# Kernel tuning notes

Measured on AMD Instinct MI355X. Metric: run time of the kernel, lower is better.

Reference implementation:

```python
import jax, jax.numpy as jnp
import numpy as np

# EEACSF hyperparameters (module defaults)
CUTOFF = 5.2
ANG_CUTOFF = 3.5
RADIAL_ETA = 16.0
ANGULAR_ETA = 8.0
RDIV = 16          # radial_dist_divisions
ADIV = 4           # angular_dist_divisions
ZETA = 32.0
SECTIONS = 4       # angle_sections
R_START = 0.8
A_START = 0.8
N_SPECIES = 87     # size of periodic-table / valence table

N_ATOMS = 20000
N_EDGES = 640000       # radial edges
N_ANG_EDGES = 160000   # angular-graph edges
N_PAIRS = 560000       # angle pairs


def setup_inputs() -> dict:
    key = jax.random.key(0)
    ks = jax.random.split(key, 12)
    species = jax.random.randint(ks[0], (N_ATOMS,), 0, N_SPECIES)
    # radial graph: distances in (R_START, CUTOFF)
    distances = R_START + (CUTOFF - R_START) * jax.random.uniform(ks[1], (N_EDGES,), jnp.float32)
    switch = jax.random.uniform(ks[2], (N_EDGES,), jnp.float32)
    edge_src = jax.random.randint(ks[3], (N_EDGES,), 0, N_ATOMS)
    edge_dst = jax.random.randint(ks[4], (N_EDGES,), 0, N_ATOMS)
    # angular graph
    ang_angles = np.pi * jax.random.uniform(ks[5], (N_PAIRS,), jnp.float32)
    ang_distances = A_START + (ANG_CUTOFF - A_START) * jax.random.uniform(ks[6], (N_ANG_EDGES,), jnp.float32)
    ang_switch = jax.random.uniform(ks[7], (N_ANG_EDGES,), jnp.float32)
    ang_edge_dst = jax.random.randint(ks[8], (N_ANG_EDGES,), 0, N_ATOMS)
    angle_src = jax.random.randint(ks[9], (N_PAIRS,), 0, N_ANG_EDGES)
    angle_dst = jax.random.randint(ks[10], (N_PAIRS,), 0, N_ANG_EDGES)
    central_atom = jax.random.randint(ks[11], (N_PAIRS,), 0, N_ATOMS)
    # valence structure table (stands in for the preprocessed VALENCE_STRUCTURE constant)
    valence_table = jax.random.uniform(jax.random.fold_in(key, 99), (N_SPECIES, 4), jnp.float32)
    return {
        "species": species, "distances": distances, "switch": switch,
        "edge_src": edge_src, "edge_dst": edge_dst,
        "ang_angles": ang_angles, "ang_distances": ang_distances,
        "ang_switch": ang_switch, "ang_edge_dst": ang_edge_dst,
        "angle_src": angle_src, "angle_dst": angle_dst,
        "central_atom": central_atom, "valence_table": valence_table,
    }


def reference(species, distances, switch, edge_src, edge_dst,
              ang_angles, ang_distances, ang_switch, ang_edge_dst,
              angle_src, angle_dst, central_atom, valence_table):
    n_atoms = species.shape[0]
    valence = valence_table[species]                                  # [N,4]

    # ---- radial AEV ----
    shiftR = jnp.asarray(np.linspace(R_START, CUTOFF, RDIV + 1)[None, :-1], distances.dtype)
    x2 = RADIAL_ETA * (distances[:, None] - shiftR) ** 2              # [E,16]
    radial_terms = 0.25 * jnp.exp(-x2) * switch[:, None]              # [E,16]
    radial_aev = jax.ops.segment_sum(
        radial_terms[:, :, None] * valence[edge_dst, None, :],        # [E,16,4]
        edge_src, num_segments=n_atoms,
    ).reshape(n_atoms, -1)                                            # [N,64]

    # ---- angular AEV ----
    d12 = 0.5 * (ang_distances[angle_src] + ang_distances[angle_dst])[:, None]  # [P,1]
    angle_start = np.pi / (2 * SECTIONS)
    shiftZ = jnp.asarray((np.linspace(0, np.pi, SECTIONS + 1) + angle_start)[None, :-1], ang_distances.dtype)
    shiftA = jnp.asarray(np.linspace(A_START, ANG_CUTOFF, ADIV + 1)[None, :-1], ang_distances.dtype)
    factor1 = (0.5 + 0.5 * jnp.cos(ang_angles[:, None] - shiftZ)) ** ZETA       # [P,4]
    factor2 = jnp.exp(-ANGULAR_ETA * (d12 - shiftA) ** 2)                       # [P,4]
    angular_terms = (factor1[:, None, :] * factor2[:, :, None]).reshape(-1, SECTIONS * ADIV)
    angular_terms = angular_terms * 2 * (ang_switch[angle_src] * ang_switch[angle_dst])[:, None]  # [P,16]

    valence_dst = valence[ang_edge_dst]                               # [E2,4]
    vp = valence_dst[angle_src] + valence_dst[angle_dst]              # [P,4]
    vm = valence_dst[angle_src] * valence_dst[angle_dst]              # [P,4]
    valence_ang = (vp[:, :, None] * vm[:, None, :]).reshape(-1, 16)   # [P,16]

    angular_aev = jax.ops.segment_sum(
        angular_terms[:, :, None] * valence_ang[:, None, :],          # [P,16,16]
        central_atom, num_segments=n_atoms,
    ).reshape(n_atoms, -1)                                            # [N,256]

    onehot = jax.nn.one_hot(species, N_SPECIES, dtype=distances.dtype)  # [N,87]
    return jnp.concatenate((onehot, radial_aev, angular_aev), axis=-1)  # [N,407]
```

## Files before the change

kernel.cpp:

```cpp
#include <hip/hip_runtime.h>
#include <hip/hip_fp16.h>
#include <math.h>

#define NCOLS   407
#define RAD_OFF 87
#define ANG_OFF 151
#define T1      2048
#define WB      32
#define MAXBKT  640
#define CAPF    1792


typedef __attribute__((ext_vector_type(8))) _Float16 f16x8;
typedef __attribute__((ext_vector_type(4))) float    f32x4;

static __device__ inline unsigned pack2(float a, float b) {
    __half2 h = __floats2half2_rn(a, b);
    return *reinterpret_cast<unsigned*>(&h);
}
static __device__ inline float2 unpack2(unsigned u) {
    __half2 h = *reinterpret_cast<__half2*>(&u);
    return __half22float2(h);
}

__global__ __launch_bounds__(256) void ze_kernel(const float* __restrict__ ang_dist,
                                                 const float* __restrict__ ang_sw,
                                                 const int* __restrict__ ang_edge_dst,
                                                 const int* __restrict__ species,
                                                 const float4* __restrict__ valence,
                                                 uint4* __restrict__ edata,
                                                 int* __restrict__ cursors,
                                                 int n_ang_edges, int nb_edata) {
    int bid = blockIdx.x;
    int t = threadIdx.x;
    if (bid == nb_edata) {
        for (int i = t; i < 2 * MAXBKT; i += 256) cursors[i] = 0;
        return;
    }
    int i = bid * 2560 + t;
    #pragma unroll
    for (int k = 0; k < 10; ++k, i += 256) {
        if (i < n_ang_edges) {
            float4 v = valence[species[ang_edge_dst[i]]];
            uint4 r;
            r.x = __float_as_uint(ang_dist[i]);
            r.y = __float_as_uint(ang_sw[i]);
            r.z = pack2(v.x, v.y);
            r.w = pack2(v.z, v.w);
            edata[i] = r;
        }
    }
}

__global__ __launch_bounds__(256) void pass1_kernel(
    const float* __restrict__ dist, const float* __restrict__ sw,
    const int* __restrict__ esrc, const int* __restrict__ edst,
    const float* __restrict__ ang_angles,
    const int* __restrict__ psrc, const int* __restrict__ pdst,
    const int* __restrict__ central,
    const int* __restrict__ species, const float4* __restrict__ valence,
    int* __restrict__ cur_rad, int* __restrict__ cur_ang,
    uint4* __restrict__ arr_rad, uint4* __restrict__ arr_ang,
    int n_edges, int n_pairs, int nbkt, int nt_rad)
{
    __shared__ uint4 buf[T1];
    __shared__ int   lh[MAXBKT];
    __shared__ int   gb[MAXBKT];
    __shared__ int   sc[256];

    int bid = blockIdx.x;
    int t = threadIdx.x;
    int is_ang = bid >= nt_rad;
    const int* key = is_ang ? central : esrc;
    int* cursor = is_ang ? cur_ang : cur_rad;
    int n   = is_ang ? n_pairs : n_edges;
    int off = (is_ang ? bid - nt_rad : bid) * T1;
    int cnt = min(T1, n - off);
    uint4* arr = is_ang ? arr_ang : arr_rad;

    for (int b = t; b < nbkt; b += 256) lh[b] = 0;
    __syncthreads();

    int meta[T1 / 256];
    #pragma unroll
    for (int k = 0; k < T1 / 256; ++k) {
        int i = off + k * 256 + t;
        meta[k] = -1;
        if (i < n) {
            int b = key[i] >> 5;
            int r = atomicAdd(&lh[b], 1);
            meta[k] = (b << 12) | r;
        }
    }
    __syncthreads();

    {
        int ch = (nbkt + 255) >> 8;
        int vals[4];
        int lo2 = t * ch, s = 0;
        for (int k = 0; k < ch; ++k) {
            int idx = lo2 + k;
            int v = (idx < nbkt) ? lh[idx] : 0;
            vals[k] = v; s += v;
        }
        sc[t] = s;
        __syncthreads();
        for (int o = 1; o < 256; o <<= 1) {
            int v = (t >= o) ? sc[t - o] : 0;
            __syncthreads();
            sc[t] += v;
            __syncthreads();
        }
        int run = sc[t] - s;
        for (int k = 0; k < ch; ++k) {
            int idx = lo2 + k;
            if (idx < nbkt) {
                lh[idx] = run;
                if (vals[k] > 0)
                    gb[idx] = idx * CAPF + atomicAdd(&cursor[idx], vals[k]);
            }
            run += vals[k];
        }
        __syncthreads();
    }

    #pragma unroll
    for (int k = 0; k < T1 / 256; ++k) {
        if (meta[k] < 0) continue;
        int i = off + k * 256 + t;
        int b = meta[k] >> 12, r = meta[k] & 4095;
        uint4 rec;
        if (!is_ang) {
            float d  = dist[i];
            float ps = 0.25f * sw[i];
            float4 v = valence[species[edst[i]]];
            rec.x = __float_as_uint(d);
            rec.y = pack2(ps * v.x, ps * v.y);
            rec.z = pack2(ps * v.z, ps * v.w);
            rec.w = (unsigned)esrc[i];
        } else {
            rec.x = (unsigned)psrc[i];
            rec.y = (unsigned)pdst[i];
            rec.z = __float_as_uint(ang_angles[i]);
            rec.w = (unsigned)central[i];
        }
        buf[lh[b] + r] = rec;
    }
    __syncthreads();

    #pragma unroll
    for (int k = 0; k < T1 / 256; ++k) {
        int j = k * 256 + t;
        if (j < cnt) {
            uint4 r = buf[j];
            int b = (int)(r.w >> 5);
            int gpos = gb[b] + (j - lh[b]);
            if (gpos < (b + 1) * CAPF) arr[gpos] = r;
        }
    }
}

__global__ __launch_bounds__(256) void pass2B_kernel(
    const uint4* __restrict__ arr_rad, const uint4* __restrict__ arr_ang,
    const uint4* __restrict__ edata,
    const int* __restrict__ cur_rad, const int* __restrict__ cur_ang,
    const int* __restrict__ species,
    float* __restrict__ out, int nbkt, int n_atoms)
{
    __shared__ uint4 buf[CAPF];
    __shared__ unsigned short ord[CAPF];
    __shared__ int lh[WB];
    __shared__ int sA[WB + 1];
    __shared__ uint4 stg[4][256];

    int bid = blockIdx.x;
    int t = threadIdx.x;
    int g = bid >= nbkt;
    int b = g ? bid - nbkt : bid;
    int lo  = b * CAPF;
    int cnt = min(g ? cur_ang[b] : cur_rad[b], CAPF);
    const uint4* arr = g ? arr_ang : arr_rad;
    int loA = b << 5;

    if (t < WB) lh[t] = 0;
    __syncthreads();
    for (int j = t; j < cnt; j += 256) {
        uint4 r = arr[lo + j];
        buf[j] = r;
        int a = (int)r.w - loA;
        if ((unsigned)a < WB) atomicAdd(&lh[a], 1);
    }
    __syncthreads();
    if (t == 0) {
        int run = 0;
        for (int a = 0; a < WB; ++a) { sA[a] = run; run += lh[a]; }
        sA[WB] = run;
    }
    __syncthreads();
    if (t < WB) lh[t] = sA[t];
    __syncthreads();
    for (int j = t; j < cnt; j += 256) {
        int a = (int)buf[j].w - loA;
        if ((unsigned)a < WB) {
            int pos = atomicAdd(&lh[a], 1);
            ord[pos] = (unsigned short)j;
        }
    }
    __syncthreads();

    int w    = t >> 6;
    int lane = t & 63;
    int m  = lane & 15;
    int g4 = lane >> 4;

    if (g) {
        const _Float16* hl = (const _Float16*)stg[w];
        for (int ai = 0; ai < 8; ++ai) {
            int a = w * 8 + ai;
            int atom = loA + a;
            if (atom >= n_atoms) break;
            int beg = sA[a], end = sA[a + 1];
            f32x4 acc = {0.f, 0.f, 0.f, 0.f};

            for (int base = beg; base < end; base += 64) {
                int idx = base + lane;
                unsigned q[16];
                if (idx < end) {
                    uint4 pr = buf[ord[idx]];
                    int e1 = (int)pr.x;
                    int e2 = (int)pr.y;
                    float ang = __uint_as_float(pr.z);
                    uint4 r1 = edata[e1];
                    uint4 r2 = edata[e2];
                    float d12 = 0.5f * (__uint_as_float(r1.x) + __uint_as_float(r2.x));
                    float swp = 2.0f * __uint_as_float(r1.y) * __uint_as_float(r2.y);
                    float2 v1a = unpack2(r1.z), v1b = unpack2(r1.w);
                    float2 v2a = unpack2(r2.z), v2b = unpack2(r2.w);
                    float vp[4] = {v1a.x + v2a.x, v1a.y + v2a.y, v1b.x + v2b.x, v1b.y + v2b.y};
                    float vm[4] = {v1a.x * v2a.x, v1a.y * v2a.y, v1b.x * v2b.x, v1b.y * v2b.y};

                    float sa, ca;
                    __sincosf(ang, &sa, &ca);
                    const float czv[4] = { 0.92387953f,  0.38268343f, -0.38268343f, -0.92387953f };
                    const float szv[4] = { 0.38268343f,  0.92387953f,  0.92387953f,  0.38268343f };
                    float f1v[4];
                    #pragma unroll
                    for (int z = 0; z < 4; ++z) {
                        float y = 0.5f + 0.5f * (ca * czv[z] + sa * szv[z]);
                        float y2 = y * y, y4 = y2 * y2, y8 = y4 * y4, y16 = y8 * y8;
                        f1v[z] = y16 * y16;
                    }
                    float f2sv[4];
                    #pragma unroll
                    for (int aa = 0; aa < 4; ++aa) {
                        float x = d12 - (0.8f + 0.675f * (float)aa);
                        f2sv[aa] = swp * __expf(-8.0f * x * x);
                    }
                    #pragma unroll
                    for (int aa = 0; aa < 4; ++aa) {
                        q[aa * 2 + 0] = pack2(f2sv[aa] * f1v[0], f2sv[aa] * f1v[1]);
                        q[aa * 2 + 1] = pack2(f2sv[aa] * f1v[2], f2sv[aa] * f1v[3]);
                    }
                    #pragma unroll
                    for (int i2 = 0; i2 < 4; ++i2) {
                        q[8 + i2 * 2 + 0] = pack2(vp[i2] * vm[0], vp[i2] * vm[1]);
                        q[8 + i2 * 2 + 1] = pack2(vp[i2] * vm[2], vp[i2] * vm[3]);
                    }
                } else {
                    #pragma unroll
                    for (int k = 0; k < 16; ++k) q[k] = 0u;
                }
                stg[w][lane * 4 + 0] = make_uint4(q[0],  q[1],  q[2],  q[3]);
                stg[w][lane * 4 + 1] = make_uint4(q[4],  q[5],  q[6],  q[7]);
                stg[w][lane * 4 + 2] = make_uint4(q[8],  q[9],  q[10], q[11]);
                stg[w][lane * 4 + 3] = make_uint4(q[12], q[13], q[14], q[15]);
                asm volatile("s_waitcnt lgkmcnt(0)" ::: "memory");

                int cc = min(64, end - base);
                {
                    f16x8 wf, uf;
                    #pragma unroll
                    for (int i = 0; i < 8; ++i) {
                        int row = (g4 << 3) + i;
                        wf[i] = hl[row * 32 + m];
                        uf[i] = hl[row * 32 + 16 + m];
                    }
                    acc = __builtin_amdgcn_mfma_f32_16x16x32_f16(wf, uf, acc, 0, 0, 0);
                }
                if (cc > 32) {
                    f16x8 wf, uf;
                    #pragma unroll
                    for (int i = 0; i < 8; ++i) {
                        int row = 32 + (g4 << 3) + i;
                        wf[i] = hl[row * 32 + m];
                        uf[i] = hl[row * 32 + 16 + m];
                    }
                    acc = __builtin_amdgcn_mfma_f32_16x16x32_f16(wf, uf, acc, 0, 0, 0);
                }
                asm volatile("s_waitcnt lgkmcnt(0)" ::: "memory");
            }
            float* orow = out + (size_t)atom * NCOLS + ANG_OFF;
            #pragma unroll
            for (int r = 0; r < 4; ++r)
                orow[(g4 * 4 + r) * 16 + m] = acc[r];
        }
        return;
    }

    const _Float16* hl = (const _Float16*)buf;
    const float*    fl = (const float*)buf;
    float shiftm = 0.8f + 0.275f * (float)m;
    for (int ai = 0; ai < 8; ++ai) {
        int a = w * 8 + ai;
        int atom = loA + a;
        if (atom >= n_atoms) break;
        int beg = sA[a], end = sA[a + 1];
        f32x4 acc = {0.f, 0.f, 0.f, 0.f};

        for (int base = beg; base < end; base += 64) {
            int cnt2 = min(64, end - base);
            {
                f16x8 wf, uf;
                #pragma unroll
                for (int i = 0; i < 8; ++i) {
                    int k = (g4 << 3) + i;
                    int live = (k < cnt2);
                    int o = live ? (int)ord[base + k] : 0;
                    float d = fl[o * 4];
                    float x = d - shiftm;
                    float e = __expf(-16.0f * x * x);
                    wf[i] = live ? (_Float16)e : (_Float16)0.0f;
                    uf[i] = (live && m < 4) ? hl[o * 8 + 2 + m] : (_Float16)0.0f;
                }
                acc = __builtin_amdgcn_mfma_f32_16x16x32_f16(wf, uf, acc, 0, 0, 0);
            }
            if (cnt2 > 32) {
                f16x8 wf, uf;
                #pragma unroll
                for (int i = 0; i < 8; ++i) {
                    int k = 32 + (g4 << 3) + i;
                    int live = (k < cnt2);
                    int o = live ? (int)ord[base + k] : 0;
                    float d = fl[o * 4];
                    float x = d - shiftm;
                    float e = __expf(-16.0f * x * x);
                    wf[i] = live ? (_Float16)e : (_Float16)0.0f;
                    uf[i] = (live && m < 4) ? hl[o * 8 + 2 + m] : (_Float16)0.0f;
                }
                acc = __builtin_amdgcn_mfma_f32_16x16x32_f16(wf, uf, acc, 0, 0, 0);
            }
        }
        if (m < 4) {
            size_t rowbase = (size_t)atom * NCOLS;
            #pragma unroll
            for (int r = 0; r < 4; ++r)
                out[rowbase + RAD_OFF + (g4 * 4 + r) * 4 + m] = acc[r];
        }
    }

    for (int idx2 = t; idx2 < WB * 87; idx2 += 256) {
        int a = idx2 / 87, c = idx2 - a * 87;
        int atom = loA + a;
        if (atom < n_atoms)
            out[(size_t)atom * NCOLS + c] = (c == species[atom]) ? 1.0f : 0.0f;
    }
}

extern "C" void kernel_launch(void* const* d_in, const int* in_sizes, int n_in,
                              void* d_out, int out_size, void* d_ws, size_t ws_size,
                              hipStream_t stream) {
    const int*   species      = (const int*)  d_in[0];
    const float* distances    = (const float*)d_in[1];
    const float* switch_      = (const float*)d_in[2];
    const int*   edge_src     = (const int*)  d_in[3];
    const int*   edge_dst     = (const int*)  d_in[4];
    const float* ang_angles   = (const float*)d_in[5];
    const float* ang_dist     = (const float*)d_in[6];
    const float* ang_switch   = (const float*)d_in[7];
    const int*   ang_edge_dst = (const int*)  d_in[8];
    const int*   angle_src    = (const int*)  d_in[9];
    const int*   angle_dst    = (const int*)  d_in[10];
    const int*   central_atom = (const int*)  d_in[11];
    const float4* valence     = (const float4*)d_in[12];

    float* out = (float*)d_out;

    const int n_atoms     = in_sizes[0];
    const int n_edges     = in_sizes[1];
    const int n_ang_edges = in_sizes[6];
    const int n_pairs     = in_sizes[5];

    const int nbkt   = (n_atoms + WB - 1) / WB;
    const int nt_rad = (n_edges + T1 - 1) / T1;
    const int nt_ang = (n_pairs + T1 - 1) / T1;

    char* ws = (char*)d_ws;
    size_t off = 0;
    auto alloc = [&](size_t bytes) -> void* {
        void* p = ws + off;
        off = (off + bytes + 15) & ~(size_t)15;
        return p;
    };
    uint4* arr_rad = (uint4*)alloc((size_t)nbkt * CAPF * 16);
    uint4* arr_ang = (uint4*)alloc((size_t)nbkt * CAPF * 16);
    uint4* edata   = (uint4*)alloc((size_t)n_ang_edges * 16);
    int*   cursors = (int*)  alloc((size_t)2 * MAXBKT * sizeof(int));
    int* cur_rad = cursors;
    int* cur_ang = cursors + MAXBKT;

    int nb_edata = (n_ang_edges + 2559) / 2560;
    ze_kernel<<<nb_edata + 1, 256, 0, stream>>>(
        ang_dist, ang_switch, ang_edge_dst, species, valence,
        edata, cursors, n_ang_edges, nb_edata);

    pass1_kernel<<<nt_rad + nt_ang, 256, 0, stream>>>(
        distances, switch_, edge_src, edge_dst,
        ang_angles, angle_src, angle_dst, central_atom,
        species, valence, cur_rad, cur_ang, arr_rad, arr_ang,
        n_edges, n_pairs, nbkt, nt_rad);

    pass2B_kernel<<<2 * nbkt, 256, 0, stream>>>(
        arr_rad, arr_ang, edata, cur_rad, cur_ang, species, out, nbkt, n_atoms);
}
```

Before: 84.65 us.

## Precompute radial edge records in prologue kernel; use wave-shuffle scans in bucketing

Moves the radial edge feature packing (distance, switch-scaled valence gathered through species) out of the scatter pass into the first kernel, so pass1 only reads a precomputed 16-byte record. The pass1 bucket scan is replaced with a wavefront shuffle scan plus a cross-wave fixup, which removes the many block barriers of the shared-memory scan. pass1's tile grows to 3072 items per block. In pass2B the second atomic pass and the serial per-atom scan are replaced by per-thread ranks and a shuffle scan. The cost is an extra 16-byte-per-edge intermediate written and read back through global memory.

```diff
diff --git a/kernel.cpp b/kernel.cpp
--- a/kernel.cpp
+++ b/kernel.cpp
@@ -5,10 +5,12 @@
 #define NCOLS   407
 #define RAD_OFF 87
 #define ANG_OFF 151
-#define T1      2048
+#define T1      3072
+#define KPT     (T1 / 256)
 #define WB      32
 #define MAXBKT  640
 #define CAPF    1792
+#define C2      (CAPF / 256)
 
 
 typedef __attribute__((ext_vector_type(8))) _Float16 f16x8;
@@ -26,39 +28,61 @@
 __global__ __launch_bounds__(256) void ze_kernel(const float* __restrict__ ang_dist,
                                                  const float* __restrict__ ang_sw,
                                                  const int* __restrict__ ang_edge_dst,
+                                                 const float* __restrict__ dist,
+                                                 const float* __restrict__ sw,
+                                                 const int* __restrict__ edst,
                                                  const int* __restrict__ species,
                                                  const float4* __restrict__ valence,
                                                  uint4* __restrict__ edata,
+                                                 uint4* __restrict__ rad_edata,
                                                  int* __restrict__ cursors,
-                                                 int n_ang_edges, int nb_edata) {
+                                                 int n_ang_edges, int n_edges,
+                                                 int nbe, int nbr) {
     int bid = blockIdx.x;
     int t = threadIdx.x;
-    if (bid == nb_edata) {
+    if (bid == nbe + nbr) {
         for (int i = t; i < 2 * MAXBKT; i += 256) cursors[i] = 0;
         return;
     }
-    int i = bid * 2560 + t;
-    #pragma unroll
-    for (int k = 0; k < 10; ++k, i += 256) {
-        if (i < n_ang_edges) {
-            float4 v = valence[species[ang_edge_dst[i]]];
-            uint4 r;
-            r.x = __float_as_uint(ang_dist[i]);
-            r.y = __float_as_uint(ang_sw[i]);
-            r.z = pack2(v.x, v.y);
-            r.w = pack2(v.z, v.w);
-            edata[i] = r;
+    if (bid < nbe) {
+        int i = bid * 2560 + t;
+        #pragma unroll
+        for (int k = 0; k < 10; ++k, i += 256) {
+            if (i < n_ang_edges) {
+                float4 v = valence[species[ang_edge_dst[i]]];
+                uint4 r;
+                r.x = __float_as_uint(ang_dist[i]);
+                r.y = __float_as_uint(ang_sw[i]);
+                r.z = pack2(v.x, v.y);
+                r.w = pack2(v.z, v.w);
+                edata[i] = r;
+            }
+        }
+    } else {
+        int i = (bid - nbe) * 2560 + t;
+        #pragma unroll
+        for (int k = 0; k < 10; ++k, i += 256) {
+            if (i < n_edges) {
+                float d  = dist[i];
+                float ps = 0.25f * sw[i];
+                float4 v = valence[species[edst[i]]];
+                uint4 r;
+                r.x = __float_as_uint(d);
+                r.y = pack2(ps * v.x, ps * v.y);
+                r.z = pack2(ps * v.z, ps * v.w);
+                r.w = 0u;
+                rad_edata[i] = r;
+            }
         }
     }
 }
 
 __global__ __launch_bounds__(256) void pass1_kernel(
-    const float* __restrict__ dist, const float* __restrict__ sw,
-    const int* __restrict__ esrc, const int* __restrict__ edst,
+    const uint4* __restrict__ rad_edata,
+    const int* __restrict__ esrc,
     const float* __restrict__ ang_angles,
     const int* __restrict__ psrc, const int* __restrict__ pdst,
     const int* __restrict__ central,
-    const int* __restrict__ species, const float4* __restrict__ valence,
     int* __restrict__ cur_rad, int* __restrict__ cur_ang,
     uint4* __restrict__ arr_rad, uint4* __restrict__ arr_ang,
     int n_edges, int n_pairs, int nbkt, int nt_rad)
@@ -66,7 +90,7 @@
     __shared__ uint4 buf[T1];
     __shared__ int   lh[MAXBKT];
     __shared__ int   gb[MAXBKT];
-    __shared__ int   sc[256];
+    __shared__ int   wtot[4];
 
     int bid = blockIdx.x;
     int t = threadIdx.x;
@@ -81,75 +105,77 @@
     for (int b = t; b < nbkt; b += 256) lh[b] = 0;
     __syncthreads();
 
-    int meta[T1 / 256];
+    int meta[KPT];
     #pragma unroll
-    for (int k = 0; k < T1 / 256; ++k) {
+    for (int k = 0; k < KPT; ++k) {
         int i = off + k * 256 + t;
         meta[k] = -1;
         if (i < n) {
-            int b = key[i] >> 5;
-            int r = atomicAdd(&lh[b], 1);
-            meta[k] = (b << 12) | r;
+            int atom = key[i];
+            int r = atomicAdd(&lh[atom >> 5], 1);
+            meta[k] = (atom << 12) | r;
         }
     }
     __syncthreads();
 
     {
-        int ch = (nbkt + 255) >> 8;
-        int vals[4];
-        int lo2 = t * ch, s = 0;
-        for (int k = 0; k < ch; ++k) {
-            int idx = lo2 + k;
-            int v = (idx < nbkt) ? lh[idx] : 0;
-            vals[k] = v; s += v;
-        }
-        sc[t] = s;
+        int w = t >> 6, lane = t & 63;
+        int W4  = (nbkt + 3) >> 2;
+        int wlo = w * W4;
+        int whi = min(wlo + W4, nbkt);
+        int b0 = wlo + lane * 3;
+        int c0 = (b0     < whi) ? lh[b0]     : 0;
+        int c1 = (b0 + 1 < whi) ? lh[b0 + 1] : 0;
+        int c2 = (b0 + 2 < whi) ? lh[b0 + 2] : 0;
+        int lsum = c0 + c1 + c2;
+        int s = lsum;
+        #pragma unroll
+        for (int o = 1; o < 64; o <<= 1) {
+            int u = __shfl_up(s, o, 64);
+            if (lane >= o) s += u;
+        }
+        int excl = s - lsum;
+        if (c0) gb[b0]     = b0       * CAPF + atomicAdd(&cursor[b0],     c0);
+        if (c1) gb[b0 + 1] = (b0 + 1) * CAPF + atomicAdd(&cursor[b0 + 1], c1);
+        if (c2) gb[b0 + 2] = (b0 + 2) * CAPF + atomicAdd(&cursor[b0 + 2], c2);
+        if (b0     < whi) lh[b0]     = excl;
+        if (b0 + 1 < whi) lh[b0 + 1] = excl + c0;
+        if (b0 + 2 < whi) lh[b0 + 2] = excl + c0 + c1;
+        if (lane == 63) wtot[w] = s;
         __syncthreads();
-        for (int o = 1; o < 256; o <<= 1) {
-            int v = (t >= o) ? sc[t - o] : 0;
-            __syncthreads();
-            sc[t] += v;
-            __syncthreads();
-        }
-        int run = sc[t] - s;
-        for (int k = 0; k < ch; ++k) {
-            int idx = lo2 + k;
-            if (idx < nbkt) {
-                lh[idx] = run;
-                if (vals[k] > 0)
-                    gb[idx] = idx * CAPF + atomicAdd(&cursor[idx], vals[k]);
-            }
-            run += vals[k];
+        int wbase = 0;
+        for (int ww = 0; ww < w; ++ww) wbase += wtot[ww];
+        if (wbase) {
+            if (b0     < whi) lh[b0]     += wbase;
+            if (b0 + 1 < whi) lh[b0 + 1] += wbase;
+            if (b0 + 2 < whi) lh[b0 + 2] += wbase;
         }
         __syncthreads();
     }
 
     #pragma unroll
-    for (int k = 0; k < T1 / 256; ++k) {
+    for (int k = 0; k < KPT; ++k) {
         if (meta[k] < 0) continue;
         int i = off + k * 256 + t;
-        int b = meta[k] >> 12, r = meta[k] & 4095;
+        int atom = meta[k] >> 12, r = meta[k] & 4095;
+        int b = atom >> 5;
         uint4 rec;
         if (!is_ang) {
-            float d  = dist[i];
-            float ps = 0.25f * sw[i];
-            float4 v = valence[species[edst[i]]];
-            rec.x = __float_as_uint(d);
-            rec.y = pack2(ps * v.x, ps * v.y);
-            rec.z = pack2(ps * v.z, ps * v.w);
-            rec.w = (unsigned)esrc[i];
+            uint4 e = rad_edata[i];
+            rec.x = e.x; rec.y = e.y; rec.z = e.z;
+            rec.w = (unsigned)atom;
         } else {
             rec.x = (unsigned)psrc[i];
             rec.y = (unsigned)pdst[i];
             rec.z = __float_as_uint(ang_angles[i]);
-            rec.w = (unsigned)central[i];
+            rec.w = (unsigned)atom;
         }
         buf[lh[b] + r] = rec;
     }
     __syncthreads();
 
     #pragma unroll
-    for (int k = 0; k < T1 / 256; ++k) {
+    for (int k = 0; k < KPT; ++k) {
         int j = k * 256 + t;
         if (j < cnt) {
             uint4 r = buf[j];
@@ -184,26 +210,39 @@
 
     if (t < WB) lh[t] = 0;
     __syncthreads();
-    for (int j = t; j < cnt; j += 256) {
-        uint4 r = arr[lo + j];
-        buf[j] = r;
-        int a = (int)r.w - loA;
-        if ((unsigned)a < WB) atomicAdd(&lh[a], 1);
-    }
-    __syncthreads();
-    if (t == 0) {
-        int run = 0;
-        for (int a = 0; a < WB; ++a) { sA[a] = run; run += lh[a]; }
-        sA[WB] = run;
-    }
-    __syncthreads();
-    if (t < WB) lh[t] = sA[t];
-    __syncthreads();
-    for (int j = t; j < cnt; j += 256) {
-        int a = (int)buf[j].w - loA;
-        if ((unsigned)a < WB) {
-            int pos = atomicAdd(&lh[a], 1);
-            ord[pos] = (unsigned short)j;
+    int myar[C2];
+    #pragma unroll
+    for (int c = 0; c < C2; ++c) {
+        int j = c * 256 + t;
+        myar[c] = -1;
+        if (j < cnt) {
+            uint4 r = arr[lo + j];
+            buf[j] = r;
+            int a = (int)r.w - loA;
+            if ((unsigned)a < WB) {
+                int rk = atomicAdd(&lh[a], 1);
+                myar[c] = (a << 12) | rk;
+            }
+        }
+    }
+    __syncthreads();
+    if (t < 64) {
+        int v = (t < WB) ? lh[t] : 0;
+        int s = v;
+        #pragma unroll
+        for (int o = 1; o < WB; o <<= 1) {
+            int u = __shfl_up(s, o, 64);
+            if (t >= o) s += u;
+        }
+        if (t < WB) sA[t + 1] = s;
+        if (t == 0) sA[0] = 0;
+    }
+    __syncthreads();
+    #pragma unroll
+    for (int c = 0; c < C2; ++c) {
+        if (myar[c] >= 0) {
+            int j = c * 256 + t;
+            ord[sA[myar[c] >> 12] + (myar[c] & 4095)] = (unsigned short)j;
         }
     }
     __syncthreads();
@@ -401,22 +440,24 @@
         off = (off + bytes + 15) & ~(size_t)15;
         return p;
     };
-    uint4* arr_rad = (uint4*)alloc((size_t)nbkt * CAPF * 16);
-    uint4* arr_ang = (uint4*)alloc((size_t)nbkt * CAPF * 16);
-    uint4* edata   = (uint4*)alloc((size_t)n_ang_edges * 16);
-    int*   cursors = (int*)  alloc((size_t)2 * MAXBKT * sizeof(int));
+    uint4* arr_rad   = (uint4*)alloc((size_t)nbkt * CAPF * 16);
+    uint4* arr_ang   = (uint4*)alloc((size_t)nbkt * CAPF * 16);
+    uint4* rad_edata = (uint4*)alloc((size_t)n_edges * 16);
+    uint4* edata     = (uint4*)alloc((size_t)n_ang_edges * 16);
+    int*   cursors   = (int*)  alloc((size_t)2 * MAXBKT * sizeof(int));
     int* cur_rad = cursors;
     int* cur_ang = cursors + MAXBKT;
 
-    int nb_edata = (n_ang_edges + 2559) / 2560;
-    ze_kernel<<<nb_edata + 1, 256, 0, stream>>>(
-        ang_dist, ang_switch, ang_edge_dst, species, valence,
-        edata, cursors, n_ang_edges, nb_edata);
+    int nbe = (n_ang_edges + 2559) / 2560;
+    int nbr = (n_edges + 2559) / 2560;
+    ze_kernel<<<nbe + nbr + 1, 256, 0, stream>>>(
+        ang_dist, ang_switch, ang_edge_dst, distances, switch_, edge_dst,
+        species, valence, edata, rad_edata, cursors,
+        n_ang_edges, n_edges, nbe, nbr);
 
     pass1_kernel<<<nt_rad + nt_ang, 256, 0, stream>>>(
-        distances, switch_, edge_src, edge_dst,
-        ang_angles, angle_src, angle_dst, central_atom,
-        species, valence, cur_rad, cur_ang, arr_rad, arr_ang,
+        rad_edata, edge_src, ang_angles, angle_src, angle_dst, central_atom,
+        cur_rad, cur_ang, arr_rad, arr_ang,
         n_edges, n_pairs, nbkt, nt_rad);
 
     pass2B_kernel<<<2 * nbkt, 256, 0, stream>>>(
```

Result: faster. 80.23 us (-5.2%).
